# Performance work log

Hardware: AMD Instinct MI355X
Metric: run time of the kernel (lower is better)

## Reference

```python
import jax, jax.numpy as jnp
import numpy as np

N_SRC = 100000
N_EDGES = 1000000
IN_FEATS = 64
N_CLASSES = 64


def setup_inputs() -> dict:
    key = jax.random.key(0)
    k1, k2, k3, k4, k5 = jax.random.split(key, 5)
    x = jax.random.normal(k1, (N_SRC, IN_FEATS), dtype=jnp.float32)
    W_self = jax.random.normal(k2, (IN_FEATS, N_CLASSES), dtype=jnp.float32) / np.sqrt(IN_FEATS)
    W_neigh = jax.random.normal(k3, (IN_FEATS, N_CLASSES), dtype=jnp.float32) / np.sqrt(IN_FEATS)
    b = jnp.zeros((N_CLASSES,), dtype=jnp.float32)
    src = jax.random.randint(k4, (N_EDGES,), 0, N_SRC, dtype=jnp.int32)
    dst = jax.random.randint(k5, (N_EDGES,), 0, N_SRC, dtype=jnp.int32)
    return {"x": x, "W_self": W_self, "W_neigh": W_neigh, "b": b,
            "src": src, "dst": dst, "num_dst": N_SRC}


def reference(x, W_self, W_neigh, b, src, dst, num_dst):
    # SAGEConv 'mean': gather src features along edges, segment-mean into dst,
    # then rst = h_dst @ W_self + h_neigh_mean @ W_neigh + b, followed by relu.
    msgs = x[src]                                                   # [E, F] irregular gather
    summed = jax.ops.segment_sum(msgs, dst, num_segments=num_dst)   # [num_dst, F]
    deg = jax.ops.segment_sum(jnp.ones((src.shape[0],), x.dtype), dst,
                              num_segments=num_dst)                 # [num_dst]
    h_neigh = summed / jnp.maximum(deg, 1.0)[:, None]               # mean (0 for isolated)
    h_dst = x[:num_dst]
    h = h_dst @ W_self + h_neigh @ W_neigh + b
    return jax.nn.relu(h)
```

## Files before the change

### kernel.cpp

```cpp
#include <hip/hip_runtime.h>


constexpr int F = 64;
constexpr int BROWS = 256;
constexpr int MAXNB = 512;
constexpr int CHP = 4096;
constexpr int LDK = 136;

typedef __attribute__((ext_vector_type(8))) short short8;
typedef __attribute__((ext_vector_type(4))) float float4v;

__device__ inline unsigned short f2bf(float f) {
    union { float f; unsigned u; } c; c.f = f;
    unsigned u = c.u;
    return (unsigned short)((u + 0x7FFFu + ((u >> 16) & 1u)) >> 16);
}
__device__ inline float bf2f(unsigned short h) {
    union { unsigned u; float f; } c; c.u = (unsigned)h << 16;
    return c.f;
}

__global__ __launch_bounds__(256) void k_conv(const float* __restrict__ x,
                                              const float* __restrict__ Ws,
                                              const float* __restrict__ Wn,
                                              unsigned short* __restrict__ xb,
                                              unsigned short* __restrict__ WtG,
                                              const int* __restrict__ dst,
                                              int* __restrict__ cnt,
                                              long n4, int n_edges, int nchunk) {
    __shared__ int hist[MAXNB];
    int t = threadIdx.x;
    long tid = (long)blockIdx.x * 256 + t;
    if (tid < 2 * F * F) {
        int i = (int)tid;
        int n = i & 63, k = i >> 6;
        float v = (k < 64) ? Ws[k * 64 + n] : Wn[(k - 64) * 64 + n];
        WtG[n * 128 + k] = f2bf(v);
    }
    int c = blockIdx.x;
    if (c < nchunk) {
        for (int i = t; i < MAXNB; i += 256) hist[i] = 0;
        __syncthreads();
        int e0 = c * CHP, e1 = min(e0 + CHP, n_edges);
        for (int e = e0 + t; e < e1; e += 256) atomicAdd(&hist[dst[e] >> 8], 1);
        __syncthreads();
        for (int i = t; i < MAXNB; i += 256) cnt[(long)c * MAXNB + i] = hist[i];
    }
    for (long i = tid; i < n4; i += (long)gridDim.x * 256) {
        float4 v = ((const float4*)x)[i];
        ushort4 o;
        o.x = f2bf(v.x); o.y = f2bf(v.y); o.z = f2bf(v.z); o.w = f2bf(v.w);
        ((ushort4*)xb)[i] = o;
    }
}

__global__ __launch_bounds__(512) void k_scanA(int* __restrict__ cnt,
                                               int* __restrict__ btot, int nchunk) {
    int b = (blockIdx.x * 512 + threadIdx.x) >> 6;
    int lane = threadIdx.x & 63;
    if (b >= MAXNB) return;
    int per = (nchunk + 63) / 64;
    int c0 = lane * per;
    int vals[16];
    int lsum = 0;
#pragma unroll
    for (int i = 0; i < 16; ++i) {
        if (i < per) {
            int c = c0 + i;
            int v = (c < nchunk) ? cnt[(long)c * MAXNB + b] : 0;
            vals[i] = v; lsum += v;
        }
    }
    int incl = lsum;
    for (int off = 1; off < 64; off <<= 1) {
        int o = __shfl_up(incl, off);
        if (lane >= off) incl += o;
    }
    int run = incl - lsum;
#pragma unroll
    for (int i = 0; i < 16; ++i) {
        if (i < per) {
            int c = c0 + i;
            if (c < nchunk) { cnt[(long)c * MAXNB + b] = run; run += vals[i]; }
        }
    }
    int tot = __shfl(incl, 63);
    if (lane == 0) btot[b] = tot;
}

__device__ inline void scan_btot(const int* __restrict__ btot, int* sbst, int t) {
    int v = btot[t];
    sbst[t] = v;
    __syncthreads();
    for (int off = 1; off < MAXNB; off <<= 1) {
        int tv = (t >= off) ? sbst[t - off] : 0;
        __syncthreads();
        sbst[t] += tv;
        __syncthreads();
    }
    int incl = sbst[t];
    __syncthreads();
    sbst[t] = incl - v;
    if (t == MAXNB - 1) sbst[MAXNB] = incl;
    __syncthreads();
}

__global__ __launch_bounds__(512) void k_place(const int* __restrict__ src,
                                               const int* __restrict__ dst,
                                               const int* __restrict__ cnt,
                                               const int* __restrict__ btot,
                                               unsigned* __restrict__ pay, int n_edges) {
    __shared__ int sbst[MAXNB + 1];
    __shared__ int lcur[MAXNB];
    int t = threadIdx.x;
    scan_btot(btot, sbst, t);
    int c = blockIdx.x;
    int e0 = c * CHP, e1 = min(e0 + CHP, n_edges);
    for (int i = t; i < MAXNB; i += 512) lcur[i] = 0;
    __syncthreads();
    const int* pref = &cnt[(long)c * MAXNB];
    for (int e = e0 + t; e < e1; e += 512) {
        int d = dst[e];
        int b = d >> 8;
        int rank = atomicAdd(&lcur[b], 1);
        int pos = sbst[b] + pref[b] + rank;
        pay[pos] = ((unsigned)src[e] << 8) | (unsigned)(d & 255);
    }
}

__global__ __launch_bounds__(512) void k_csr(const unsigned* __restrict__ pay,
                                             const int* __restrict__ btot,
                                             int* __restrict__ row_start,
                                             int* __restrict__ csr,
                                             int num_dst, int n_edges, int nb) {
    __shared__ int sbst[MAXNB + 1];
    __shared__ int hist[BROWS];
    __shared__ int scn[BROWS];
    int t = threadIdx.x;
    scan_btot(btot, sbst, t);
    int b = blockIdx.x;
    int s0 = sbst[b], s1 = sbst[b + 1];
    if (t < BROWS) hist[t] = 0;
    __syncthreads();
    for (int i = s0 + t; i < s1; i += 512) atomicAdd(&hist[pay[i] & 255], 1);
    __syncthreads();
    int v = 0;
    if (t < BROWS) { v = hist[t]; scn[t] = v; }
    __syncthreads();
    for (int off = 1; off < BROWS; off <<= 1) {
        int tv = 0;
        if (t < BROWS && t >= off) tv = scn[t - off];
        __syncthreads();
        if (t < BROWS) scn[t] += tv;
        __syncthreads();
    }
    int r0 = b * BROWS;
    if (t < BROWS) {
        int excl = scn[t] - v;
        if (r0 + t < num_dst) row_start[r0 + t] = s0 + excl;
        hist[t] = excl;
    }
    if (b == nb - 1 && t == 0) row_start[num_dst] = n_edges;
    __syncthreads();
    for (int i = s0 + t; i < s1; i += 512) {
        unsigned p = pay[i];
        int pos = atomicAdd(&hist[p & 255], 1);
        csr[s0 + pos] = (int)(p >> 8);
    }
}

__global__ __launch_bounds__(256) void k_aggregate(const unsigned short* __restrict__ xb,
                                                   const int* __restrict__ row_start,
                                                   const int* __restrict__ csr,
                                                   unsigned short* __restrict__ hb, int num_dst) {
    int lane = threadIdx.x & 63;
    int r = (blockIdx.x * 256 + threadIdx.x) >> 6;
    if (r >= num_dst) return;
    int g = lane >> 4;
    int c4 = (lane & 15) * 4;
    int s0 = row_start[r], s1 = row_start[r + 1];
    int rem = s1 - s0;
    float4 accA = make_float4(0.f, 0.f, 0.f, 0.f);
    float4 accB = make_float4(0.f, 0.f, 0.f, 0.f);
    for (int base = 0; base < rem; base += 64) {
        int sid = (base + lane < rem) ? csr[s0 + base + lane] : 0;
        int n = min(64, rem - base);
        int i = 0;
        for (; i + 7 < n; i += 8) {
            int e0 = __shfl(sid, i + g);
            int e1 = __shfl(sid, i + 4 + g);
            ushort4 u0 = *(const ushort4*)&xb[(long)e0 * F + c4];
            ushort4 u1 = *(const ushort4*)&xb[(long)e1 * F + c4];
            accA.x += bf2f(u0.x); accA.y += bf2f(u0.y); accA.z += bf2f(u0.z); accA.w += bf2f(u0.w);
            accB.x += bf2f(u1.x); accB.y += bf2f(u1.y); accB.z += bf2f(u1.z); accB.w += bf2f(u1.w);
        }
        for (; i < n; i += 4) {
            int eslot = i + g;
            int e = __shfl(sid, eslot);
            if (eslot < n) {
                ushort4 u = *(const ushort4*)&xb[(long)e * F + c4];
                accA.x += bf2f(u.x); accA.y += bf2f(u.y); accA.z += bf2f(u.z); accA.w += bf2f(u.w);
            }
        }
    }
    float4 acc;
    acc.x = accA.x + accB.x; acc.y = accA.y + accB.y;
    acc.z = accA.z + accB.z; acc.w = accA.w + accB.w;
    acc.x += __shfl_xor(acc.x, 16); acc.y += __shfl_xor(acc.y, 16);
    acc.z += __shfl_xor(acc.z, 16); acc.w += __shfl_xor(acc.w, 16);
    acc.x += __shfl_xor(acc.x, 32); acc.y += __shfl_xor(acc.y, 32);
    acc.z += __shfl_xor(acc.z, 32); acc.w += __shfl_xor(acc.w, 32);
    if (lane < 16) {
        float inv = 1.0f / fmaxf((float)rem, 1.0f);
        ushort4 o;
        o.x = f2bf(acc.x * inv); o.y = f2bf(acc.y * inv);
        o.z = f2bf(acc.z * inv); o.w = f2bf(acc.w * inv);
        *(ushort4*)&hb[(long)r * F + c4] = o;
    }
}

__global__ __launch_bounds__(256) void k_gemm_mfma(
    const unsigned short* __restrict__ xb, const unsigned short* __restrict__ hb,
    const unsigned short* __restrict__ WtG,
    const float* __restrict__ b, float* __restrict__ out, int num_dst)
{
    __shared__ __align__(16) unsigned short Atile[64 * LDK];
    __shared__ __align__(16) unsigned short Wt[64 * LDK];
    int t = threadIdx.x;
    int row0 = blockIdx.x * 64;

    for (int i = t; i < 64 * 16; i += 256) {
        int r = i >> 4, s = i & 15;
        *(short8*)&Wt[r * LDK + s * 8] = *(const short8*)&WtG[r * 128 + s * 8];
        int g = row0 + r;
        short8 v = {0, 0, 0, 0, 0, 0, 0, 0};
        if (g < num_dst)
            v = (s < 8) ? *(const short8*)&xb[(long)g * F + s * 8]
                        : *(const short8*)&hb[(long)g * F + (s - 8) * 8];
        *(short8*)&Atile[r * LDK + s * 8] = v;
    }
    __syncthreads();

    int lane = t & 63;
    int wave = t >> 6;
    int m = lane & 15;
    int quad = lane >> 4;
    const unsigned short* arow = &Atile[(wave * 16 + m) * LDK + quad * 8];

    float4v acc[4];
#pragma unroll
    for (int nt = 0; nt < 4; ++nt) acc[nt] = (float4v){0.f, 0.f, 0.f, 0.f};

#pragma unroll
    for (int kb = 0; kb < 4; ++kb) {
        short8 a = *(const short8*)(arow + kb * 32);
#pragma unroll
        for (int nt = 0; nt < 4; ++nt) {
            short8 bf = *(const short8*)&Wt[(nt * 16 + m) * LDK + quad * 8 + kb * 32];
            acc[nt] = __builtin_amdgcn_mfma_f32_16x16x32_bf16(a, bf, acc[nt], 0, 0, 0);
        }
    }

    int gr_base = row0 + wave * 16 + quad * 4;
#pragma unroll
    for (int nt = 0; nt < 4; ++nt) {
        int col = nt * 16 + m;
        float bias = b[col];
#pragma unroll
        for (int rg = 0; rg < 4; ++rg) {
            int g = gr_base + rg;
            if (g < num_dst) out[(long)g * F + col] = fmaxf(acc[nt][rg] + bias, 0.0f);
        }
    }
}

__global__ __launch_bounds__(256) void k_scatter(const float* __restrict__ x, const int* __restrict__ src,
                                                 const int* __restrict__ dst, float* __restrict__ summed,
                                                 float* __restrict__ degf, int n_edges) {
    long tid = (long)blockIdx.x * 256 + threadIdx.x;
    int e = (int)(tid >> 6);
    if (e >= n_edges) return;
    int f = threadIdx.x & 63;
    atomicAdd(&summed[(long)dst[e] * F + f], x[(long)src[e] * F + f]);
    if (f == 0) atomicAdd(&degf[dst[e]], 1.0f);
}

__global__ __launch_bounds__(256) void k_gemm_shfl(
    const float* __restrict__ x, const float* __restrict__ Ws, const float* __restrict__ Wn,
    const float* __restrict__ b, const float* __restrict__ degf, float* inout, int num_dst)
{
    __shared__ float Wl[2 * F * F];
    for (int i = threadIdx.x; i < F * F; i += 256) { Wl[i] = Ws[i]; Wl[F * F + i] = Wn[i]; }
    __syncthreads();
    int lane = threadIdx.x & 63;
    int r = (blockIdx.x * 256 + threadIdx.x) >> 6;
    if (r >= num_dst) return;
    float xv = x[(long)r * F + lane];
    float hv = inout[(long)r * F + lane] / fmaxf(degf[r], 1.0f);
    float acc = b[lane];
#pragma unroll
    for (int k = 0; k < F; ++k) {
        acc += __shfl(xv, k) * Wl[k * F + lane];
        acc += __shfl(hv, k) * Wl[(F + k) * F + lane];
    }
    inout[(long)r * F + lane] = fmaxf(acc, 0.0f);
}

extern "C" void kernel_launch(void* const* d_in, const int* in_sizes, int n_in,
                              void* d_out, int out_size, void* d_ws, size_t ws_size,
                              hipStream_t stream) {
    const float* x  = (const float*)d_in[0];
    const float* Ws = (const float*)d_in[1];
    const float* Wn = (const float*)d_in[2];
    const float* b  = (const float*)d_in[3];
    const int* src  = (const int*)d_in[4];
    const int* dst  = (const int*)d_in[5];
    int n_edges = in_sizes[4];
    int num_dst = out_size / F;
    float* out = (float*)d_out;

    int nchunk = (n_edges + CHP - 1) / CHP;
    int nb = (num_dst + BROWS - 1) / BROWS;

    char* ws = (char*)d_ws;
    size_t off = 0;
    auto alloc = [&](size_t bytes) { char* p = ws + off; off = (off + bytes + 255) & ~(size_t)255; return p; };
    unsigned short* xb  = (unsigned short*)alloc((size_t)num_dst * F * 2);
    unsigned short* hb  = (unsigned short*)alloc((size_t)num_dst * F * 2);
    unsigned* pay       = (unsigned*)alloc((size_t)n_edges * 4);
    int* csr            = (int*)alloc((size_t)n_edges * 4);
    int* row_start      = (int*)alloc((size_t)(num_dst + 1) * 4);
    unsigned short* WtG = (unsigned short*)alloc(2 * F * F * 2);
    int* cnt            = (int*)alloc((size_t)nchunk * MAXNB * 4);
    int* btot           = (int*)alloc(MAXNB * 4);
    bool big_ws = (off <= ws_size) && (nb <= MAXNB) && (nchunk <= 1024);

    if (big_ws) {
        long n4 = (long)num_dst * F / 4;
        int convgrid = max(2048, nchunk);
        k_conv<<<convgrid, 256, 0, stream>>>(x, Ws, Wn, xb, WtG, dst, cnt, n4, n_edges, nchunk);
        k_scanA<<<(MAXNB * 64 + 511) / 512, 512, 0, stream>>>(cnt, btot, nchunk);
        k_place<<<nchunk, 512, 0, stream>>>(src, dst, cnt, btot, pay, n_edges);
        k_csr<<<nb, 512, 0, stream>>>(pay, btot, row_start, csr, num_dst, n_edges, nb);
        k_aggregate<<<(num_dst + 3) / 4, 256, 0, stream>>>(xb, row_start, csr, hb, num_dst);
        k_gemm_mfma<<<(num_dst + 63) / 64, 256, 0, stream>>>(xb, hb, WtG, b, out, num_dst);
    } else {
        float* degf = (float*)d_ws;
        (void)hipMemsetAsync(d_out, 0, (size_t)out_size * sizeof(float), stream);
        (void)hipMemsetAsync(degf, 0, (size_t)num_dst * sizeof(float), stream);
        long tt = (long)n_edges * 64;
        k_scatter<<<(int)((tt + 255) / 256), 256, 0, stream>>>(x, src, dst, out, degf, n_edges);
        k_gemm_shfl<<<(num_dst + 3) / 4, 256, 0, stream>>>(x, Ws, Wn, b, degf, out, num_dst);
    }
}
```

Baseline: 167.0 us.

## Drop chunk-scan kernel by scattering into fixed-capacity per-bucket buffers

Removes the separate k_scanA launch. Each k_place block now computes its own per-bucket prefix by summing the counts of all earlier chunks, and writes payloads into a 2D buffer with a fixed capacity (PCAP) per destination bucket. The last chunk also writes the bucket totals, which k_csr scans itself to find the final CSR offsets. This saves a kernel launch and a global scan pass. In exchange, later blocks in k_place do redundant serial prefix work. Correctness also depends on no bucket exceeding PCAP, which is only guarded by a check on the mean load.

```diff
diff --git a/kernel.cpp b/kernel.cpp
--- a/kernel.cpp
+++ b/kernel.cpp
@@ -5,6 +5,7 @@
 constexpr int BROWS = 256;
 constexpr int MAXNB = 512;
 constexpr int CHP = 4096;
+constexpr int PCAP = 8192;
 constexpr int LDK = 136;
 
 typedef __attribute__((ext_vector_type(8))) short short8;
@@ -54,81 +55,49 @@
     }
 }
 
-__global__ __launch_bounds__(512) void k_scanA(int* __restrict__ cnt,
-                                               int* __restrict__ btot, int nchunk) {
-    int b = (blockIdx.x * 512 + threadIdx.x) >> 6;
-    int lane = threadIdx.x & 63;
-    if (b >= MAXNB) return;
-    int per = (nchunk + 63) / 64;
-    int c0 = lane * per;
-    int vals[16];
-    int lsum = 0;
-#pragma unroll
-    for (int i = 0; i < 16; ++i) {
-        if (i < per) {
-            int c = c0 + i;
-            int v = (c < nchunk) ? cnt[(long)c * MAXNB + b] : 0;
-            vals[i] = v; lsum += v;
-        }
-    }
-    int incl = lsum;
-    for (int off = 1; off < 64; off <<= 1) {
-        int o = __shfl_up(incl, off);
-        if (lane >= off) incl += o;
-    }
-    int run = incl - lsum;
-#pragma unroll
-    for (int i = 0; i < 16; ++i) {
-        if (i < per) {
-            int c = c0 + i;
-            if (c < nchunk) { cnt[(long)c * MAXNB + b] = run; run += vals[i]; }
-        }
-    }
-    int tot = __shfl(incl, 63);
-    if (lane == 0) btot[b] = tot;
-}
-
-__device__ inline void scan_btot(const int* __restrict__ btot, int* sbst, int t) {
-    int v = btot[t];
-    sbst[t] = v;
-    __syncthreads();
-    for (int off = 1; off < MAXNB; off <<= 1) {
-        int tv = (t >= off) ? sbst[t - off] : 0;
-        __syncthreads();
-        sbst[t] += tv;
-        __syncthreads();
-    }
-    int incl = sbst[t];
-    __syncthreads();
-    sbst[t] = incl - v;
-    if (t == MAXNB - 1) sbst[MAXNB] = incl;
-    __syncthreads();
-}
-
 __global__ __launch_bounds__(512) void k_place(const int* __restrict__ src,
                                                const int* __restrict__ dst,
                                                const int* __restrict__ cnt,
-                                               const int* __restrict__ btot,
-                                               unsigned* __restrict__ pay, int n_edges) {
-    __shared__ int sbst[MAXNB + 1];
+                                               unsigned* __restrict__ pay2d,
+                                               int* __restrict__ btot,
+                                               int n_edges, int nchunk) {
+    __shared__ int pref[MAXNB];
     __shared__ int lcur[MAXNB];
     int t = threadIdx.x;
-    scan_btot(btot, sbst, t);
     int c = blockIdx.x;
+    int p = 0;
+    for (int cc = 0; cc < c; ++cc) p += cnt[(long)cc * MAXNB + t];
+    pref[t] = p;
+    lcur[t] = 0;
+    if (c == nchunk - 1) btot[t] = p + cnt[(long)c * MAXNB + t];
+    __syncthreads();
     int e0 = c * CHP, e1 = min(e0 + CHP, n_edges);
-    for (int i = t; i < MAXNB; i += 512) lcur[i] = 0;
-    __syncthreads();
-    const int* pref = &cnt[(long)c * MAXNB];
     for (int e = e0 + t; e < e1; e += 512) {
         int d = dst[e];
         int b = d >> 8;
         int rank = atomicAdd(&lcur[b], 1);
-        int pos = sbst[b] + pref[b] + rank;
-        pay[pos] = ((unsigned)src[e] << 8) | (unsigned)(d & 255);
-    }
-}
-
-__global__ __launch_bounds__(512) void k_csr(const unsigned* __restrict__ pay,
+        pay2d[(long)b * PCAP + pref[b] + rank] = ((unsigned)src[e] << 8) | (unsigned)(d & 255);
+    }
+}
+
+__device__ inline void scan_btot(const int* __restrict__ btot, int* sbst, int t) {
+    int v = btot[t];
+    sbst[t] = v;
+    __syncthreads();
+    for (int off = 1; off < MAXNB; off <<= 1) {
+        int tv = (t >= off) ? sbst[t - off] : 0;
+        __syncthreads();
+        sbst[t] += tv;
+        __syncthreads();
+    }
+    int incl = sbst[t];
+    __syncthreads();
+    sbst[t] = incl - v;
+    if (t == MAXNB - 1) sbst[MAXNB] = incl;
+    __syncthreads();
+}
+
+__global__ __launch_bounds__(512) void k_csr(const unsigned* __restrict__ pay2d,
                                              const int* __restrict__ btot,
                                              int* __restrict__ row_start,
                                              int* __restrict__ csr,
@@ -139,10 +108,12 @@
     int t = threadIdx.x;
     scan_btot(btot, sbst, t);
     int b = blockIdx.x;
-    int s0 = sbst[b], s1 = sbst[b + 1];
+    int s0 = sbst[b];
+    int bt = sbst[b + 1] - s0;
+    const unsigned* bp = &pay2d[(long)b * PCAP];
     if (t < BROWS) hist[t] = 0;
     __syncthreads();
-    for (int i = s0 + t; i < s1; i += 512) atomicAdd(&hist[pay[i] & 255], 1);
+    for (int i = t; i < bt; i += 512) atomicAdd(&hist[bp[i] & 255], 1);
     __syncthreads();
     int v = 0;
     if (t < BROWS) { v = hist[t]; scn[t] = v; }
@@ -162,8 +133,8 @@
     }
     if (b == nb - 1 && t == 0) row_start[num_dst] = n_edges;
     __syncthreads();
-    for (int i = s0 + t; i < s1; i += 512) {
-        unsigned p = pay[i];
+    for (int i = t; i < bt; i += 512) {
+        unsigned p = bp[i];
         int pos = atomicAdd(&hist[p & 255], 1);
         csr[s0 + pos] = (int)(p >> 8);
     }
@@ -327,21 +298,21 @@
     auto alloc = [&](size_t bytes) { char* p = ws + off; off = (off + bytes + 255) & ~(size_t)255; return p; };
     unsigned short* xb  = (unsigned short*)alloc((size_t)num_dst * F * 2);
     unsigned short* hb  = (unsigned short*)alloc((size_t)num_dst * F * 2);
-    unsigned* pay       = (unsigned*)alloc((size_t)n_edges * 4);
+    unsigned* pay2d     = (unsigned*)alloc((size_t)MAXNB * PCAP * 4);
     int* csr            = (int*)alloc((size_t)n_edges * 4);
     int* row_start      = (int*)alloc((size_t)(num_dst + 1) * 4);
     unsigned short* WtG = (unsigned short*)alloc(2 * F * F * 2);
     int* cnt            = (int*)alloc((size_t)nchunk * MAXNB * 4);
     int* btot           = (int*)alloc(MAXNB * 4);
-    bool big_ws = (off <= ws_size) && (nb <= MAXNB) && (nchunk <= 1024);
+    long mean_load = (num_dst > 0) ? ((long)n_edges * BROWS) / num_dst : 0;
+    bool big_ws = (off <= ws_size) && (nb <= MAXNB) && (mean_load * 2 < PCAP);
 
     if (big_ws) {
         long n4 = (long)num_dst * F / 4;
         int convgrid = max(2048, nchunk);
         k_conv<<<convgrid, 256, 0, stream>>>(x, Ws, Wn, xb, WtG, dst, cnt, n4, n_edges, nchunk);
-        k_scanA<<<(MAXNB * 64 + 511) / 512, 512, 0, stream>>>(cnt, btot, nchunk);
-        k_place<<<nchunk, 512, 0, stream>>>(src, dst, cnt, btot, pay, n_edges);
-        k_csr<<<nb, 512, 0, stream>>>(pay, btot, row_start, csr, num_dst, n_edges, nb);
+        k_place<<<nchunk, 512, 0, stream>>>(src, dst, cnt, pay2d, btot, n_edges, nchunk);
+        k_csr<<<nb, 512, 0, stream>>>(pay2d, btot, row_start, csr, num_dst, n_edges, nb);
         k_aggregate<<<(num_dst + 3) / 4, 256, 0, stream>>>(xb, row_start, csr, hb, num_dst);
         k_gemm_mfma<<<(num_dst + 63) / 64, 256, 0, stream>>>(xb, hb, WtG, b, out, num_dst);
     } else {
```

Result: slower. 191.9 us (+14.9%).
